# Optimization experiments

Hardware: AMD Instinct MI355X
Metric: run time of the kernel (lower is better)

## Reference

```python
import jax, jax.numpy as jnp
import numpy as np

B, T, H, L = 64, 2048, 256, 16


def setup_inputs() -> dict:
    key = jax.random.key(0)
    ks = jax.random.split(key, 6)
    x = jax.random.normal(ks[0], (B, T, H), dtype=jnp.float32)
    tags = jax.random.randint(ks[1], (B, T), 0, L).astype(jnp.int32)
    mask = jnp.ones((B, T), dtype=bool)  # torchcrf requires mask[:,0] all on
    W = jax.random.normal(ks[2], (L, H), dtype=jnp.float32) * (1.0 / np.sqrt(H))
    b = jnp.zeros((L,), dtype=jnp.float32)
    # torchcrf initializes transitions ~ U(-0.1, 0.1)
    start_transitions = jax.random.uniform(ks[3], (L,), minval=-0.1, maxval=0.1)
    end_transitions = jax.random.uniform(ks[4], (L,), minval=-0.1, maxval=0.1)
    transitions = jax.random.uniform(ks[5], (L, L), minval=-0.1, maxval=0.1)
    return {"x": x, "W": W, "b": b,
            "start_transitions": start_transitions,
            "end_transitions": end_transitions,
            "transitions": transitions,
            "tags": tags, "mask": mask}


def reference(x, W, b, start_transitions, end_transitions, transitions, tags, mask):
    # Emitter: Linear(hidden_dim -> num_labels)
    emissions = jnp.einsum('bth,lh->btl', x, W) + b  # [B,T,L]
    maskf = mask.astype(emissions.dtype)             # [B,T]

    # ---- numerator: score of the gold tag path (vectorized, no scan) ----
    emit_gold = jnp.take_along_axis(emissions, tags[..., None].astype(jnp.int32), axis=2)[..., 0]  # [B,T]
    first_tags = tags[:, 0]
    score = start_transitions[first_tags] + emit_gold[:, 0]
    trans_gold = transitions[tags[:, :-1], tags[:, 1:]]  # [B,T-1]
    score = score + jnp.sum((trans_gold + emit_gold[:, 1:]) * maskf[:, 1:], axis=1)
    seq_ends = jnp.sum(mask.astype(jnp.int32), axis=1) - 1  # index of last valid step
    last_tags = jnp.take_along_axis(tags, seq_ends[:, None], axis=1)[:, 0]
    score = score + end_transitions[last_tags]

    # ---- denominator: forward algorithm (log partition) via lax.scan over time ----
    em_t = jnp.swapaxes(emissions, 0, 1)  # [T,B,L]
    mask_t = jnp.swapaxes(mask, 0, 1)     # [T,B]
    alpha0 = start_transitions[None, :] + em_t[0]  # [B,L]

    def step(alpha, inp):
        em, m = inp  # em: [B,L], m: [B]
        # logsumexp over previous label: alpha[b,i] + transitions[i,j] + em[b,j]
        nxt = jax.nn.logsumexp(alpha[:, :, None] + transitions[None, :, :] + em[:, None, :], axis=1)
        alpha = jnp.where(m[:, None], nxt, alpha)
        return alpha, None

    alphaT, _ = jax.lax.scan(step, alpha0, (em_t[1:], mask_t[1:]))
    denom = jax.nn.logsumexp(alphaT + end_transitions[None, :], axis=1)  # [B]

    llh = score - denom          # log-likelihood per sequence
    return -jnp.mean(llh)        # reduction='mean', nll = -crf(...)
```

## Files before the change

### kernel.cpp

```cpp
#include <hip/hip_runtime.h>
#include <math.h>


#define Bb 64
#define Tt 2048
#define Hh 256
#define Ll 16
#define CHUNK 32
#define NC (Tt / CHUNK)
#define ROWS 128
#define NCHK (ROWS / CHUNK)
#define TSTR 20

__global__ __launch_bounds__(256) void k_fused(const float* __restrict__ x,
                                               const float* __restrict__ W,
                                               const float* __restrict__ bias,
                                               const float* __restrict__ strans,
                                               const float* __restrict__ etrans,
                                               const float* __restrict__ trans,
                                               const int* __restrict__ tags,
                                               float* __restrict__ em0,
                                               float* __restrict__ Pout,
                                               float* __restrict__ lscale,
                                               float* __restrict__ score) {
  __shared__ float Wl[Ll * Hh];
  __shared__ float tile[ROWS * TSTR];
  __shared__ float trl[256];
  __shared__ float etl[256];
  __shared__ float mbuf[ROWS];
  __shared__ float bl[Ll];
  float* ghat = Wl;

  int tid = threadIdx.x;
  int b = blockIdx.x >> 4;
  int blk = blockIdx.x & 15;
  int t0 = blk * ROWS;

  for (int idx = tid; idx < Ll * Hh; idx += 256) Wl[idx] = W[idx];
  trl[tid] = trans[tid];
  etl[tid] = expf(trl[tid]);
  if (tid < Ll) bl[tid] = bias[tid];
  __syncthreads();

  int w = tid >> 6, lane = tid & 63;

  {
    int g = lane >> 2, q = lane & 3;
    int rowl = w * 32 + g;
    size_t rowg = (size_t)blockIdx.x * ROWS + rowl;
    const float4* x4 = (const float4*)x;
    float acc[2][16];
#pragma unroll
    for (int r = 0; r < 2; ++r)
#pragma unroll
      for (int l = 0; l < 16; ++l) acc[r][l] = 0.f;
    size_t rb0 = rowg * 64 + q;
    size_t rb1 = (rowg + 16) * 64 + q;

#pragma unroll 4
    for (int i = 0; i < 16; ++i) {
      float4 xv0 = x4[rb0 + i * 4];
      float4 xv1 = x4[rb1 + i * 4];
      const float* wp = Wl + i * 16 + q * 4;
#pragma unroll
      for (int l = 0; l < 16; ++l) {
        float4 wv = *(const float4*)(wp + l * Hh);
        acc[0][l] = fmaf(xv0.x, wv.x, fmaf(xv0.y, wv.y, fmaf(xv0.z, wv.z, fmaf(xv0.w, wv.w, acc[0][l]))));
        acc[1][l] = fmaf(xv1.x, wv.x, fmaf(xv1.y, wv.y, fmaf(xv1.z, wv.z, fmaf(xv1.w, wv.w, acc[1][l]))));
      }
    }
    bool qb0 = (q & 1) != 0, qb1 = (q & 2) != 0;
    float4 bq = *(const float4*)(bl + q * 4);
#pragma unroll
    for (int r = 0; r < 2; ++r) {
      float t1[16];
#pragma unroll
      for (int l = 0; l < 16; ++l) t1[l] = __shfl_xor(acc[r][l], 1);
      float r8[8];
#pragma unroll
      for (int k = 0; k < 8; ++k) r8[k] = qb0 ? (acc[r][8 + k] + t1[8 + k]) : (acc[r][k] + t1[k]);
      float t2[8];
#pragma unroll
      for (int k = 0; k < 8; ++k) t2[k] = __shfl_xor(r8[k], 2);
      float r4[4];
#pragma unroll
      for (int k = 0; k < 4; ++k) r4[k] = qb1 ? (r8[4 + k] + t2[4 + k]) : (r8[k] + t2[k]);
      float4 o = make_float4(r4[0] + bq.x, r4[1] + bq.y, r4[2] + bq.z, r4[3] + bq.w);
      *(float4*)(tile + (rowl + r * 16) * TSTR + q * 4) = o;
      if (t0 == 0 && r == 0 && tid < 4)
        *(float4*)(em0 + b * 16 + q * 4) = o;
    }
  }
  __syncthreads();

  if (tid < ROWS) {
    const float4* tp = (const float4*)(tile + tid * TSTR);
    float4 a0 = tp[0], a1 = tp[1], a2 = tp[2], a3 = tp[3];
    float m = fmaxf(fmaxf(fmaxf(fmaxf(a0.x, a0.y), fmaxf(a0.z, a0.w)),
                          fmaxf(fmaxf(a1.x, a1.y), fmaxf(a1.z, a1.w))),
                    fmaxf(fmaxf(fmaxf(a2.x, a2.y), fmaxf(a2.z, a2.w)),
                          fmaxf(fmaxf(a3.x, a3.y), fmaxf(a3.z, a3.w))));
    float4* gp = (float4*)(ghat + tid * TSTR);
    gp[0] = make_float4(expf(a0.x - m), expf(a0.y - m), expf(a0.z - m), expf(a0.w - m));
    gp[1] = make_float4(expf(a1.x - m), expf(a1.y - m), expf(a1.z - m), expf(a1.w - m));
    gp[2] = make_float4(expf(a2.x - m), expf(a2.y - m), expf(a2.z - m), expf(a2.w - m));
    gp[3] = make_float4(expf(a3.x - m), expf(a3.y - m), expf(a3.z - m), expf(a3.w - m));
    mbuf[tid] = m;
  }
  __syncthreads();

  {
    float s = 0.f;
    if (lane < 32) {
      int rl = w * 32 + lane;
      int t = t0 + rl;
      int gt = b * Tt + t;
      int tag = tags[gt];
      if (t == 0) {
        s = strans[tag] + tile[rl * TSTR + tag];
      } else {
        int pv = tags[gt - 1];
        s = trl[pv * 16 + tag] + tile[rl * TSTR + tag];
      }
      if (t == Tt - 1) s += etrans[tag];
    }
#pragma unroll
    for (int m = 1; m < 64; m <<= 1) s += __shfl_xor(s, m);
    if (lane == 0) atomicAdd(score + b, s);
  }

  {
    int i = lane >> 2, jg = lane & 3;
    int srcb = lane & ~3;
    float4 e[16];
#pragma unroll
    for (int k = 0; k < 16; ++k) e[k] = *(const float4*)(etl + k * 16 + jg * 4);

    int ci = w;
    int gc = blk * NCHK + ci;
    int sbeg = (gc == 0) ? 1 : 0;
    float off = 0.f;
    for (int s = sbeg; s < CHUNK; ++s) off += mbuf[ci * CHUNK + s];
    float4 p = make_float4(i == jg * 4 + 0 ? 1.f : 0.f, i == jg * 4 + 1 ? 1.f : 0.f,
                           i == jg * 4 + 2 ? 1.f : 0.f, i == jg * 4 + 3 ? 1.f : 0.f);
    for (int s = sbeg; s < CHUNK; ++s) {
      float4 pm0, pm1, pm2, pm3;
      pm0.x = __shfl(p.x, srcb + 0); pm0.y = __shfl(p.y, srcb + 0);
      pm0.z = __shfl(p.z, srcb + 0); pm0.w = __shfl(p.w, srcb + 0);
      pm1.x = __shfl(p.x, srcb + 1); pm1.y = __shfl(p.y, srcb + 1);
      pm1.z = __shfl(p.z, srcb + 1); pm1.w = __shfl(p.w, srcb + 1);
      pm2.x = __shfl(p.x, srcb + 2); pm2.y = __shfl(p.y, srcb + 2);
      pm2.z = __shfl(p.z, srcb + 2); pm2.w = __shfl(p.w, srcb + 2);
      pm3.x = __shfl(p.x, srcb + 3); pm3.y = __shfl(p.y, srcb + 3);
      pm3.z = __shfl(p.z, srcb + 3); pm3.w = __shfl(p.w, srcb + 3);
      float4 acc = make_float4(0.f, 0.f, 0.f, 0.f);
#define K4ACC(pmv, kb)                                                                \
      acc.x = fmaf(pmv.x, e[kb + 0].x, acc.x); acc.y = fmaf(pmv.x, e[kb + 0].y, acc.y); \
      acc.z = fmaf(pmv.x, e[kb + 0].z, acc.z); acc.w = fmaf(pmv.x, e[kb + 0].w, acc.w); \
      acc.x = fmaf(pmv.y, e[kb + 1].x, acc.x); acc.y = fmaf(pmv.y, e[kb + 1].y, acc.y); \
      acc.z = fmaf(pmv.y, e[kb + 1].z, acc.z); acc.w = fmaf(pmv.y, e[kb + 1].w, acc.w); \
      acc.x = fmaf(pmv.z, e[kb + 2].x, acc.x); acc.y = fmaf(pmv.z, e[kb + 2].y, acc.y); \
      acc.z = fmaf(pmv.z, e[kb + 2].z, acc.z); acc.w = fmaf(pmv.z, e[kb + 2].w, acc.w); \
      acc.x = fmaf(pmv.w, e[kb + 3].x, acc.x); acc.y = fmaf(pmv.w, e[kb + 3].y, acc.y); \
      acc.z = fmaf(pmv.w, e[kb + 3].z, acc.z); acc.w = fmaf(pmv.w, e[kb + 3].w, acc.w);
      K4ACC(pm0, 0) K4ACC(pm1, 4) K4ACC(pm2, 8) K4ACC(pm3, 12)
#undef K4ACC
      float4 g4 = *(const float4*)(ghat + (ci * CHUNK + s) * TSTR + jg * 4);
      p.x = acc.x * g4.x; p.y = acc.y * g4.y; p.z = acc.z * g4.z; p.w = acc.w * g4.w;
      if (((s & 7) == 7) || (s == CHUNK - 1)) {
        float mx = fmaxf(fmaxf(p.x, p.y), fmaxf(p.z, p.w));
#pragma unroll
        for (int msk = 1; msk < 64; msk <<= 1) mx = fmaxf(mx, __shfl_xor(mx, msk));
        float inv = __builtin_amdgcn_rcpf(mx);
        p.x *= inv; p.y *= inv; p.z *= inv; p.w *= inv;
        off += logf(mx);
      }
    }
    ((float4*)(Pout + ((size_t)(b * NC + gc)) * 256))[lane] = p;
    if (lane == 0) lscale[b * NC + gc] = off;
  }
}

__global__ __launch_bounds__(64) void k_combine(const float* __restrict__ em0,
                                                const float* __restrict__ P,
                                                const float* __restrict__ lscale,
                                                const float* __restrict__ strans,
                                                const float* __restrict__ etrans,
                                                float* __restrict__ denom) {
  int b = blockIdx.x, lane = threadIdx.x;
  __shared__ float Pl[NC * 256];
  const float4* src = (const float4*)(P + (size_t)b * NC * 256);
  float4* dst = (float4*)Pl;
  for (int idx = lane; idx < NC * 64; idx += 64) dst[idx] = src[idx];
  float ls = lscale[b * NC + lane];
#pragma unroll
  for (int m = 1; m < 64; m <<= 1) ls += __shfl_xor(ls, m);

  int j = lane & 15, ig = lane >> 4;
  float a = strans[j] + em0[b * 16 + j];
  float m0 = a;
#pragma unroll
  for (int m = 1; m < 16; m <<= 1) m0 = fmaxf(m0, __shfl_xor(m0, m));
  float v = expf(a - m0);
  float o = m0 + ls;
  __syncthreads();

  for (int cc = 0; cc < NC; ++cc) {
    const float* Pc = Pl + cc * 256;
    float part = 0.f;
#pragma unroll
    for (int r = 0; r < 4; ++r) {
      int srcl = (ig << 4) + ig * 4 + r;
      float vr = __shfl(v, srcl);
      part = fmaf(vr, Pc[(ig * 4 + r) * 16 + j], part);
    }
    part += __shfl_xor(part, 16);
    part += __shfl_xor(part, 32);
    if ((cc & 3) == 3) {
      float mx = part;
#pragma unroll
      for (int m = 1; m < 16; m <<= 1) mx = fmaxf(mx, __shfl_xor(mx, m));
      o += logf(mx);
      v = part * __builtin_amdgcn_rcpf(mx);
    } else {
      v = part;
    }
  }
  float sj = v * expf(etrans[j]);
#pragma unroll
  for (int m = 1; m < 16; m <<= 1) sj += __shfl_xor(sj, m);
  if (lane == 0) denom[b] = o + logf(sj);
}

__global__ __launch_bounds__(64) void k_final(const float* __restrict__ score,
                                              const float* __restrict__ denom,
                                              float* __restrict__ out) {
  int lane = threadIdx.x;
  float llh = score[lane] - denom[lane];
#pragma unroll
  for (int m = 1; m < 64; m <<= 1) llh += __shfl_xor(llh, m);
  if (lane == 0) out[0] = -llh * (1.0f / 64.0f);
}

extern "C" void kernel_launch(void* const* d_in, const int* in_sizes, int n_in,
                              void* d_out, int out_size, void* d_ws, size_t ws_size,
                              hipStream_t stream) {
  const float* x = (const float*)d_in[0];
  const float* W = (const float*)d_in[1];
  const float* bias = (const float*)d_in[2];
  const float* strans = (const float*)d_in[3];
  const float* etrans = (const float*)d_in[4];
  const float* trans = (const float*)d_in[5];
  const int* tags = (const int*)d_in[6];

  float* ws = (float*)d_ws;
  float* em0 = ws;
  float* P = em0 + Bb * 16;
  float* lscale = P + (size_t)Bb * NC * 256;
  float* score = lscale + Bb * NC;
  float* denom = score + Bb;
  float* out = (float*)d_out;

  hipMemsetAsync(score, 0, Bb * sizeof(float), stream);
  hipLaunchKernelGGL(k_fused, dim3(Bb * Tt / ROWS), dim3(256), 0, stream,
                     x, W, bias, strans, etrans, trans, tags, em0, P, lscale, score);
  hipLaunchKernelGGL(k_combine, dim3(Bb), dim3(64), 0, stream, em0, P, lscale, strans, etrans, denom);
  hipLaunchKernelGGL(k_final, dim3(1), dim3(64), 0, stream, score, denom, out);
}
```

Before: 283.0 us.

## Use bf16 MFMA for emitter GEMM and chunk transfer-matrix products

Replaces the FP32 FMA emission projection with bf16 MFMA 16x16x32 instructions, loading W fragments straight from global memory instead of staging it in LDS. The per-chunk 16x16 transfer-matrix recurrence also moves to MFMA, with bf16 exp-emission tiles and a per-wave LDS buffer used to re-pack the running product as the A operand. The combine kernel now uses 256 threads to load P into LDS, then one wave runs the scan. This cuts FP32 ALU work and LDS footprint, but introduces bf16 rounding error into both the emissions and the log-partition product.

```diff
diff --git a/kernel.cpp b/kernel.cpp
--- a/kernel.cpp
+++ b/kernel.cpp
@@ -9,8 +9,24 @@
 #define CHUNK 32
 #define NC (Tt / CHUNK)
 #define ROWS 128
-#define NCHK (ROWS / CHUNK)
 #define TSTR 20
+
+typedef __attribute__((ext_vector_type(8))) short short8;
+typedef __attribute__((ext_vector_type(4))) float f32x4;
+
+__device__ __forceinline__ unsigned pk2bf(float a, float b) {
+  unsigned ua = __float_as_uint(a) + 0x8000u;
+  unsigned ub = __float_as_uint(b) + 0x8000u;
+  return (ua >> 16) | (ub & 0xFFFF0000u);
+}
+__device__ __forceinline__ short8 pack8(float4 lo, float4 hi) {
+  union { int4 i; short8 s; } u;
+  u.i.x = pk2bf(lo.x, lo.y);
+  u.i.y = pk2bf(lo.z, lo.w);
+  u.i.z = pk2bf(hi.x, hi.y);
+  u.i.w = pk2bf(hi.z, hi.w);
+  return u.s;
+}
 
 __global__ __launch_bounds__(256) void k_fused(const float* __restrict__ x,
                                                const float* __restrict__ W,
@@ -23,175 +39,146 @@
                                                float* __restrict__ Pout,
                                                float* __restrict__ lscale,
                                                float* __restrict__ score) {
-  __shared__ float Wl[Ll * Hh];
   __shared__ float tile[ROWS * TSTR];
-  __shared__ float trl[256];
-  __shared__ float etl[256];
-  __shared__ float mbuf[ROWS];
-  __shared__ float bl[Ll];
-  float* ghat = Wl;
-
-  int tid = threadIdx.x;
-  int b = blockIdx.x >> 4;
-  int blk = blockIdx.x & 15;
-  int t0 = blk * ROWS;
-
-  for (int idx = tid; idx < Ll * Hh; idx += 256) Wl[idx] = W[idx];
-  trl[tid] = trans[tid];
-  etl[tid] = expf(trl[tid]);
-  if (tid < Ll) bl[tid] = bias[tid];
+  __shared__ unsigned short ghb[ROWS * 16];
+  __shared__ float Pbuf[4][16 * TSTR];
+
+  const int tid = threadIdx.x, w = tid >> 6, lane = tid & 63;
+  const int n = lane & 15, quad = lane >> 4;
+  const int b = blockIdx.x >> 4, blk = blockIdx.x & 15;
+  const int gc = blk * 4 + w;
+
+  {
+    const float4* wp4 = (const float4*)(W + (size_t)n * Hh) + quad * 2;
+    short8 Bf[8];
+#pragma unroll
+    for (int ks = 0; ks < 8; ++ks) Bf[ks] = pack8(wp4[ks * 8], wp4[ks * 8 + 1]);
+    float bs = bias[n];
+    size_t Grow = (size_t)blockIdx.x * ROWS + w * 32 + n;
+    const float4* xa = (const float4*)(x + Grow * Hh) + quad * 2;
+    const float4* xb = (const float4*)(x + (Grow + 16) * Hh) + quad * 2;
+    f32x4 acc0 = {0.f, 0.f, 0.f, 0.f}, acc1 = {0.f, 0.f, 0.f, 0.f};
+#pragma unroll
+    for (int ks = 0; ks < 8; ++ks) {
+      short8 a0 = pack8(xa[ks * 8], xa[ks * 8 + 1]);
+      short8 a1 = pack8(xb[ks * 8], xb[ks * 8 + 1]);
+      acc0 = __builtin_amdgcn_mfma_f32_16x16x32_bf16(a0, Bf[ks], acc0, 0, 0, 0);
+      acc1 = __builtin_amdgcn_mfma_f32_16x16x32_bf16(a1, Bf[ks], acc1, 0, 0, 0);
+    }
+#pragma unroll
+    for (int r = 0; r < 4; ++r) {
+      tile[(w * 32 + quad * 4 + r) * TSTR + n] = acc0[r] + bs;
+      tile[(w * 32 + 16 + quad * 4 + r) * TSTR + n] = acc1[r] + bs;
+    }
+    if (blk == 0 && w == 0 && quad == 0) em0[b * 16 + n] = acc0[0] + bs;
+  }
   __syncthreads();
 
-  int w = tid >> 6, lane = tid & 63;
-
-  {
-    int g = lane >> 2, q = lane & 3;
-    int rowl = w * 32 + g;
-    size_t rowg = (size_t)blockIdx.x * ROWS + rowl;
-    const float4* x4 = (const float4*)x;
-    float acc[2][16];
-#pragma unroll
-    for (int r = 0; r < 2; ++r)
-#pragma unroll
-      for (int l = 0; l < 16; ++l) acc[r][l] = 0.f;
-    size_t rb0 = rowg * 64 + q;
-    size_t rb1 = (rowg + 16) * 64 + q;
-
-#pragma unroll 4
-    for (int i = 0; i < 16; ++i) {
-      float4 xv0 = x4[rb0 + i * 4];
-      float4 xv1 = x4[rb1 + i * 4];
-      const float* wp = Wl + i * 16 + q * 4;
-#pragma unroll
-      for (int l = 0; l < 16; ++l) {
-        float4 wv = *(const float4*)(wp + l * Hh);
-        acc[0][l] = fmaf(xv0.x, wv.x, fmaf(xv0.y, wv.y, fmaf(xv0.z, wv.z, fmaf(xv0.w, wv.w, acc[0][l]))));
-        acc[1][l] = fmaf(xv1.x, wv.x, fmaf(xv1.y, wv.y, fmaf(xv1.z, wv.z, fmaf(xv1.w, wv.w, acc[1][l]))));
-      }
-    }
-    bool qb0 = (q & 1) != 0, qb1 = (q & 2) != 0;
-    float4 bq = *(const float4*)(bl + q * 4);
-#pragma unroll
-    for (int r = 0; r < 2; ++r) {
-      float t1[16];
-#pragma unroll
-      for (int l = 0; l < 16; ++l) t1[l] = __shfl_xor(acc[r][l], 1);
-      float r8[8];
-#pragma unroll
-      for (int k = 0; k < 8; ++k) r8[k] = qb0 ? (acc[r][8 + k] + t1[8 + k]) : (acc[r][k] + t1[k]);
-      float t2[8];
-#pragma unroll
-      for (int k = 0; k < 8; ++k) t2[k] = __shfl_xor(r8[k], 2);
-      float r4[4];
-#pragma unroll
-      for (int k = 0; k < 4; ++k) r4[k] = qb1 ? (r8[4 + k] + t2[4 + k]) : (r8[k] + t2[k]);
-      float4 o = make_float4(r4[0] + bq.x, r4[1] + bq.y, r4[2] + bq.z, r4[3] + bq.w);
-      *(float4*)(tile + (rowl + r * 16) * TSTR + q * 4) = o;
-      if (t0 == 0 && r == 0 && tid < 4)
-        *(float4*)(em0 + b * 16 + q * 4) = o;
-    }
-  }
-  __syncthreads();
-
-  if (tid < ROWS) {
-    const float4* tp = (const float4*)(tile + tid * TSTR);
-    float4 a0 = tp[0], a1 = tp[1], a2 = tp[2], a3 = tp[3];
-    float m = fmaxf(fmaxf(fmaxf(fmaxf(a0.x, a0.y), fmaxf(a0.z, a0.w)),
-                          fmaxf(fmaxf(a1.x, a1.y), fmaxf(a1.z, a1.w))),
-                    fmaxf(fmaxf(fmaxf(a2.x, a2.y), fmaxf(a2.z, a2.w)),
-                          fmaxf(fmaxf(a3.x, a3.y), fmaxf(a3.z, a3.w))));
-    float4* gp = (float4*)(ghat + tid * TSTR);
-    gp[0] = make_float4(expf(a0.x - m), expf(a0.y - m), expf(a0.z - m), expf(a0.w - m));
-    gp[1] = make_float4(expf(a1.x - m), expf(a1.y - m), expf(a1.z - m), expf(a1.w - m));
-    gp[2] = make_float4(expf(a2.x - m), expf(a2.y - m), expf(a2.z - m), expf(a2.w - m));
-    gp[3] = make_float4(expf(a3.x - m), expf(a3.y - m), expf(a3.z - m), expf(a3.w - m));
-    mbuf[tid] = m;
-  }
-  __syncthreads();
-
-  {
-    float s = 0.f;
+  {
+    float s2 = 0.f;
     if (lane < 32) {
       int rl = w * 32 + lane;
-      int t = t0 + rl;
+      int t = blk * ROWS + rl;
       int gt = b * Tt + t;
       int tag = tags[gt];
-      if (t == 0) {
-        s = strans[tag] + tile[rl * TSTR + tag];
-      } else {
-        int pv = tags[gt - 1];
-        s = trl[pv * 16 + tag] + tile[rl * TSTR + tag];
-      }
-      if (t == Tt - 1) s += etrans[tag];
-    }
-#pragma unroll
-    for (int m = 1; m < 64; m <<= 1) s += __shfl_xor(s, m);
-    if (lane == 0) atomicAdd(score + b, s);
-  }
-
-  {
-    int i = lane >> 2, jg = lane & 3;
-    int srcb = lane & ~3;
-    float4 e[16];
-#pragma unroll
-    for (int k = 0; k < 16; ++k) e[k] = *(const float4*)(etl + k * 16 + jg * 4);
-
-    int ci = w;
-    int gc = blk * NCHK + ci;
-    int sbeg = (gc == 0) ? 1 : 0;
-    float off = 0.f;
-    for (int s = sbeg; s < CHUNK; ++s) off += mbuf[ci * CHUNK + s];
-    float4 p = make_float4(i == jg * 4 + 0 ? 1.f : 0.f, i == jg * 4 + 1 ? 1.f : 0.f,
-                           i == jg * 4 + 2 ? 1.f : 0.f, i == jg * 4 + 3 ? 1.f : 0.f);
+      float ev = tile[rl * TSTR + tag];
+      if (t == 0) s2 = strans[tag] + ev;
+      else        s2 = trans[tags[gt - 1] * 16 + tag] + ev;
+      if (t == Tt - 1) s2 += etrans[tag];
+    }
+#pragma unroll
+    for (int msk = 1; msk < 64; msk <<= 1) s2 += __shfl_xor(s2, msk);
+    if (lane == 0) atomicAdd(score + b, s2);
+  }
+
+  float offsum = 0.f;
+  {
+    if (lane < 32) {
+      int rl = w * 32 + lane;
+      const float4* tp = (const float4*)(tile + rl * TSTR);
+      float4 a0 = tp[0], a1 = tp[1], a2 = tp[2], a3 = tp[3];
+      float m = fmaxf(fmaxf(fmaxf(fmaxf(a0.x, a0.y), fmaxf(a0.z, a0.w)),
+                            fmaxf(fmaxf(a1.x, a1.y), fmaxf(a1.z, a1.w))),
+                      fmaxf(fmaxf(fmaxf(a2.x, a2.y), fmaxf(a2.z, a2.w)),
+                            fmaxf(fmaxf(a3.x, a3.y), fmaxf(a3.z, a3.w))));
+      float4 e0 = make_float4(expf(a0.x - m), expf(a0.y - m), expf(a0.z - m), expf(a0.w - m));
+      float4 e1 = make_float4(expf(a1.x - m), expf(a1.y - m), expf(a1.z - m), expf(a1.w - m));
+      float4 e2 = make_float4(expf(a2.x - m), expf(a2.y - m), expf(a2.z - m), expf(a2.w - m));
+      float4 e3 = make_float4(expf(a3.x - m), expf(a3.y - m), expf(a3.z - m), expf(a3.w - m));
+      int4 lo, hi;
+      lo.x = pk2bf(e0.x, e0.y); lo.y = pk2bf(e0.z, e0.w);
+      lo.z = pk2bf(e1.x, e1.y); lo.w = pk2bf(e1.z, e1.w);
+      hi.x = pk2bf(e2.x, e2.y); hi.y = pk2bf(e2.z, e2.w);
+      hi.z = pk2bf(e3.x, e3.y); hi.w = pk2bf(e3.z, e3.w);
+      ((int4*)ghb)[rl * 2] = lo;
+      ((int4*)ghb)[rl * 2 + 1] = hi;
+      int t = blk * ROWS + rl;
+      offsum = (t >= 1) ? m : 0.f;
+    }
+#pragma unroll
+    for (int msk = 1; msk < 64; msk <<= 1) offsum += __shfl_xor(offsum, msk);
+  }
+  __syncthreads();
+
+  {
+    short8 Eb = {0, 0, 0, 0, 0, 0, 0, 0};
+    if (quad < 2) {
+      float e[8];
+#pragma unroll
+      for (int j = 0; j < 8; ++j) e[j] = expf(trans[(quad * 8 + j) * 16 + n]);
+      Eb = pack8(make_float4(e[0], e[1], e[2], e[3]), make_float4(e[4], e[5], e[6], e[7]));
+    }
+    short8 Aid = {0, 0, 0, 0, 0, 0, 0, 0};
+    if (quad < 2 && (n >> 3) == quad) ((short*)&Aid)[n & 7] = (short)0x3F80;
+
+    float* Pw = Pbuf[w];
+    float off = offsum;
+    const int sbeg = (gc == 0) ? 1 : 0;
+    const unsigned short* grow = ghb + (w * 32) * 16 + n;
+    short8 A = Aid;
     for (int s = sbeg; s < CHUNK; ++s) {
-      float4 pm0, pm1, pm2, pm3;
-      pm0.x = __shfl(p.x, srcb + 0); pm0.y = __shfl(p.y, srcb + 0);
-      pm0.z = __shfl(p.z, srcb + 0); pm0.w = __shfl(p.w, srcb + 0);
-      pm1.x = __shfl(p.x, srcb + 1); pm1.y = __shfl(p.y, srcb + 1);
-      pm1.z = __shfl(p.z, srcb + 1); pm1.w = __shfl(p.w, srcb + 1);
-      pm2.x = __shfl(p.x, srcb + 2); pm2.y = __shfl(p.y, srcb + 2);
-      pm2.z = __shfl(p.z, srcb + 2); pm2.w = __shfl(p.w, srcb + 2);
-      pm3.x = __shfl(p.x, srcb + 3); pm3.y = __shfl(p.y, srcb + 3);
-      pm3.z = __shfl(p.z, srcb + 3); pm3.w = __shfl(p.w, srcb + 3);
-      float4 acc = make_float4(0.f, 0.f, 0.f, 0.f);
-#define K4ACC(pmv, kb)                                                                \
-      acc.x = fmaf(pmv.x, e[kb + 0].x, acc.x); acc.y = fmaf(pmv.x, e[kb + 0].y, acc.y); \
-      acc.z = fmaf(pmv.x, e[kb + 0].z, acc.z); acc.w = fmaf(pmv.x, e[kb + 0].w, acc.w); \
-      acc.x = fmaf(pmv.y, e[kb + 1].x, acc.x); acc.y = fmaf(pmv.y, e[kb + 1].y, acc.y); \
-      acc.z = fmaf(pmv.y, e[kb + 1].z, acc.z); acc.w = fmaf(pmv.y, e[kb + 1].w, acc.w); \
-      acc.x = fmaf(pmv.z, e[kb + 2].x, acc.x); acc.y = fmaf(pmv.z, e[kb + 2].y, acc.y); \
-      acc.z = fmaf(pmv.z, e[kb + 2].z, acc.z); acc.w = fmaf(pmv.z, e[kb + 2].w, acc.w); \
-      acc.x = fmaf(pmv.w, e[kb + 3].x, acc.x); acc.y = fmaf(pmv.w, e[kb + 3].y, acc.y); \
-      acc.z = fmaf(pmv.w, e[kb + 3].z, acc.z); acc.w = fmaf(pmv.w, e[kb + 3].w, acc.w);
-      K4ACC(pm0, 0) K4ACC(pm1, 4) K4ACC(pm2, 8) K4ACC(pm3, 12)
-#undef K4ACC
-      float4 g4 = *(const float4*)(ghat + (ci * CHUNK + s) * TSTR + jg * 4);
-      p.x = acc.x * g4.x; p.y = acc.y * g4.y; p.z = acc.z * g4.z; p.w = acc.w * g4.w;
+      f32x4 z = {0.f, 0.f, 0.f, 0.f};
+      f32x4 d = __builtin_amdgcn_mfma_f32_16x16x32_bf16(A, Eb, z, 0, 0, 0);
+      float g = __uint_as_float(((unsigned)grow[s * 16]) << 16);
+      d[0] *= g; d[1] *= g; d[2] *= g; d[3] *= g;
       if (((s & 7) == 7) || (s == CHUNK - 1)) {
-        float mx = fmaxf(fmaxf(p.x, p.y), fmaxf(p.z, p.w));
+        float mx = fmaxf(fmaxf(d[0], d[1]), fmaxf(d[2], d[3]));
 #pragma unroll
         for (int msk = 1; msk < 64; msk <<= 1) mx = fmaxf(mx, __shfl_xor(mx, msk));
         float inv = __builtin_amdgcn_rcpf(mx);
-        p.x *= inv; p.y *= inv; p.z *= inv; p.w *= inv;
+        d[0] *= inv; d[1] *= inv; d[2] *= inv; d[3] *= inv;
         off += logf(mx);
       }
-    }
-    ((float4*)(Pout + ((size_t)(b * NC + gc)) * 256))[lane] = p;
-    if (lane == 0) lscale[b * NC + gc] = off;
-  }
-}
-
-__global__ __launch_bounds__(64) void k_combine(const float* __restrict__ em0,
-                                                const float* __restrict__ P,
-                                                const float* __restrict__ lscale,
-                                                const float* __restrict__ strans,
-                                                const float* __restrict__ etrans,
-                                                float* __restrict__ denom) {
-  int b = blockIdx.x, lane = threadIdx.x;
+#pragma unroll
+      for (int r = 0; r < 4; ++r) Pw[(quad * 4 + r) * TSTR + n] = d[r];
+      if (quad < 2) {
+        const float4* pr = (const float4*)(Pw + n * TSTR + quad * 8);
+        A = pack8(pr[0], pr[1]);
+      }
+    }
+    {
+      int i = lane >> 2, jg = lane & 3;
+      float4 pv = *(const float4*)(Pw + i * TSTR + jg * 4);
+      ((float4*)(Pout + ((size_t)(b * NC + gc)) * 256))[lane] = pv;
+      if (lane == 0) lscale[b * NC + gc] = off;
+    }
+  }
+}
+
+__global__ __launch_bounds__(256) void k_combine(const float* __restrict__ em0,
+                                                 const float* __restrict__ P,
+                                                 const float* __restrict__ lscale,
+                                                 const float* __restrict__ strans,
+                                                 const float* __restrict__ etrans,
+                                                 float* __restrict__ denom) {
+  int b = blockIdx.x, tid = threadIdx.x;
   __shared__ float Pl[NC * 256];
   const float4* src = (const float4*)(P + (size_t)b * NC * 256);
   float4* dst = (float4*)Pl;
-  for (int idx = lane; idx < NC * 64; idx += 64) dst[idx] = src[idx];
+  for (int idx = tid; idx < NC * 64; idx += 256) dst[idx] = src[idx];
+  __syncthreads();
+  if (tid >= 64) return;
+  int lane = tid;
   float ls = lscale[b * NC + lane];
 #pragma unroll
   for (int m = 1; m < 64; m <<= 1) ls += __shfl_xor(ls, m);
@@ -203,7 +190,6 @@
   for (int m = 1; m < 16; m <<= 1) m0 = fmaxf(m0, __shfl_xor(m0, m));
   float v = expf(a - m0);
   float o = m0 + ls;
-  __syncthreads();
 
   for (int cc = 0; cc < NC; ++cc) {
     const float* Pc = Pl + cc * 256;
@@ -264,6 +250,6 @@
   hipMemsetAsync(score, 0, Bb * sizeof(float), stream);
   hipLaunchKernelGGL(k_fused, dim3(Bb * Tt / ROWS), dim3(256), 0, stream,
                      x, W, bias, strans, etrans, trans, tags, em0, P, lscale, score);
-  hipLaunchKernelGGL(k_combine, dim3(Bb), dim3(64), 0, stream, em0, P, lscale, strans, etrans, denom);
+  hipLaunchKernelGGL(k_combine, dim3(Bb), dim3(256), 0, stream, em0, P, lscale, strans, etrans, denom);
   hipLaunchKernelGGL(k_final, dim3(1), dim3(64), 0, stream, score, denom, out);
 }
```

Result: faster. 243.1 us (-14.1%).
